# Kernel optimization log

Hardware: AMD Instinct MI355X
Metric: run time of the kernel (lower is better)

Reference implementation:

```python
import jax, jax.numpy as jnp
import numpy as np

B, T, C = 8, 2048, 512   # batch, seq_len, channels (= output_size for residual)
H, K, D = 4, 128, 128    # heads, key_size, per-head value size
KS, DIL = 4, 4           # conv kernel size, dilation = kernal_size**block_id
BAND = 3                 # matrix_band_part num_lower = num_upper = 3
NEG = -10000000.0


def setup_inputs() -> dict:
    key = jax.random.key(0)
    ks = jax.random.split(key, 12)
    s = 0.02
    f32 = jnp.float32
    x = jax.random.normal(ks[0], (B, T, C), f32)
    # per-head q/k/v dense params (stacked over head axis)
    Wq = jax.random.normal(ks[1], (H, C, K), f32) * s
    bq = jnp.zeros((H, K), f32)
    Wk = jax.random.normal(ks[2], (H, C, K), f32) * s
    bk = jnp.zeros((H, K), f32)
    Wv = jax.random.normal(ks[3], (H, C, D), f32) * s
    bv = jnp.zeros((H, D), f32)
    # output combiner Dense(output_size)
    Wo = jax.random.normal(ks[4], (H * D, C), f32) * s
    bo = jnp.zeros((C,), f32)
    # causal dilated Conv1D: kernel layout WIO = (kernel, in, out)
    Wc = jax.random.normal(ks[5], (KS, C, C), f32) * s
    bc = jnp.zeros((C,), f32)
    return {"x": x, "Wq": Wq, "bq": bq, "Wk": Wk, "bk": bk,
            "Wv": Wv, "bv": bv, "Wo": Wo, "bo": bo, "Wc": Wc, "bc": bc}


def reference(x, Wq, bq, Wk, bk, Wv, bv, Wo, bo, Wc, bc):
    # per-head projections: [B,H,T,K/D]
    q = jnp.einsum('btc,hck->bhtk', x, Wq) + bq[None, :, None, :]
    k = jnp.einsum('btc,hck->bhtk', x, Wk) + bk[None, :, None, :]
    v = jnp.einsum('btc,hcd->bhtd', x, Wv) + bv[None, :, None, :]
    # dense scores then band mask (faithful to matrix_band_part + abs>0 mask)
    sim = jnp.einsum('bhtk,bhsk->bhts', q, k) / jnp.sqrt(jnp.float32(K))
    idx = jnp.arange(T)
    band = (jnp.abs(idx[:, None] - idx[None, :]) <= BAND).astype(sim.dtype)
    simb = sim * band
    mask = jnp.where(jnp.abs(simb) > 0.0, 0.0, 1.0).astype(sim.dtype)
    att = jax.nn.softmax(simb + NEG * mask, axis=-1)
    heads = jnp.einsum('bhts,bhsd->bhtd', att, v)          # [B,H,T,D]
    cat = heads.transpose(0, 2, 1, 3).reshape(B, T, H * D)  # concat heads
    out = cat @ Wo + bo                                     # Dense(512)
    # causal dilated conv + relu
    pad = (KS - 1) * DIL
    conv = jax.lax.conv_general_dilated(
        out, Wc, window_strides=(1,), padding=[(pad, 0)],
        rhs_dilation=(DIL,), dimension_numbers=('NWC', 'WIO', 'NWC'))
    conv = jax.nn.relu(conv + bc)
    res = conv + x
    return jnp.where(res >= 0, res, 0.2 * res)  # leaky_relu(alpha=0.2)
```

## Files before the change

### kernel.cpp

```cpp
#include <hip/hip_runtime.h>
#include <math.h>

#define Bb    8
#define Tseq  2048
#define Cch   512
#define Mrows 16384
#define Nqkv  1536

typedef __bf16 bf16x8 __attribute__((ext_vector_type(8)));
typedef __bf16 bf16x4 __attribute__((ext_vector_type(4)));
typedef float  f32x4  __attribute__((ext_vector_type(4)));

__device__ __forceinline__ void gld_lds16(const void* g, void* l) {
  __builtin_amdgcn_global_load_lds(
      (const __attribute__((address_space(1))) unsigned int*)g,
      (__attribute__((address_space(3))) unsigned int*)l, 16, 0, 0);
}

#define SWZ(r, g) (((r) << 6) + ((((g) ^ ((r) & 7))) << 3))


__global__ __launch_bounds__(256, 4) void gemm_qkv_wp_kernel(
    const __bf16* __restrict__ xb, const __bf16* __restrict__ Wqkv_t,
    const float* __restrict__ bq, const float* __restrict__ bk,
    const float* __restrict__ bv, __bf16* __restrict__ qkv,
    const __bf16* __restrict__ Wc_t, const __bf16* __restrict__ Wob,
    __bf16* __restrict__ Wp_bt) {
  __shared__ __align__(16) __bf16 As[64 * 64];
  __shared__ __align__(16) __bf16 Bs[128 * 64];
  const int tid = threadIdx.x;
  const int w = tid >> 6, lane = tid & 63;
  const int wm = w & 1, wn = w >> 1;
  const int lm = lane & 15, quad = lane >> 4;
  const int srow = lane >> 3;
  const int scol = (((lane & 7) ^ srow) << 3);
  const int lid = blockIdx.x;

  const __bf16 *Ap, *Bp;
  __bf16* op;
  int lda, ldo, m0, n0;
  bool dobias;
  if (lid < 3072) {
    const int xcd = lid & 7, chunk = lid >> 3;
    const int idx = xcd * 384 + chunk;
    const int mt = idx / 12, nt = idx - mt * 12;
    m0 = mt * 64; n0 = nt * 128;
    Ap = xb; lda = 512; Bp = Wqkv_t;
    op = qkv; ldo = 1536; dobias = true;
  } else {
    const int l2 = lid - 3072;
    const int z = l2 >> 5;
    const int rest = l2 & 31;
    m0 = (rest >> 2) * 64;
    n0 = (rest & 3) * 128;
    Ap = Wc_t + z * 512; lda = 2048; Bp = Wob;
    op = Wp_bt + z * 512; ldo = 2048; dobias = false;
  }

  f32x4 acc[2][4] = {};
  for (int k0 = 0; k0 < 512; k0 += 64) {
#pragma unroll
    for (int it = 0; it < 2; ++it) {
      const int c = w * 2 + it;
      const int row = c * 8 + srow;
      gld_lds16(Ap + (size_t)(m0 + row) * lda + k0 + scol, &As[c * 512]);
    }
#pragma unroll
    for (int it = 0; it < 4; ++it) {
      const int c = w * 4 + it;
      const int row = c * 8 + srow;
      gld_lds16(Bp + (size_t)(n0 + row) * 512 + k0 + scol, &Bs[c * 512]);
    }
    __syncthreads();
#pragma unroll
    for (int ks = 0; ks < 2; ++ks) {
      bf16x8 af[2], bfr[4];
#pragma unroll
      for (int i = 0; i < 2; ++i)
        af[i] = *(const bf16x8*)&As[SWZ(wm * 32 + i * 16 + lm, ks * 4 + quad)];
#pragma unroll
      for (int j = 0; j < 4; ++j)
        bfr[j] = *(const bf16x8*)&Bs[SWZ(wn * 64 + j * 16 + lm, ks * 4 + quad)];
#pragma unroll
      for (int i = 0; i < 2; ++i)
#pragma unroll
        for (int j = 0; j < 4; ++j)
          acc[i][j] = __builtin_amdgcn_mfma_f32_16x16x32_bf16(af[i], bfr[j], acc[i][j], 0, 0, 0);
    }
    __syncthreads();
  }
#pragma unroll
  for (int j = 0; j < 4; ++j) {
    const int col = n0 + wn * 64 + j * 16 + lm;
    float bias = 0.f;
    if (dobias) {
      const int s = col >> 9;
      const float* bp = (s == 0) ? bq : (s == 1 ? bk : bv);
      bias = bp[col & 511];
    }
#pragma unroll
    for (int i = 0; i < 2; ++i) {
      const int row0 = m0 + wm * 32 + i * 16 + quad * 4;
#pragma unroll
      for (int r = 0; r < 4; ++r)
        op[(size_t)(row0 + r) * ldo + col] = (__bf16)(acc[i][j][r] + bias);
    }
  }
}

__global__ __launch_bounds__(256, 4) void conv_gemm_kernel(
    const __bf16* __restrict__ A,
    const __bf16* __restrict__ Bt,
    const float* __restrict__ bc, const float* __restrict__ bj,
    const float* __restrict__ x, float* __restrict__ out,
    const __bf16* __restrict__ zeros) {
  __shared__ __align__(16) __bf16 As[64 * 64];
  __shared__ __align__(16) __bf16 Bs[128 * 64];
  const int tid = threadIdx.x;
  const int w = tid >> 6, lane = tid & 63;
  const int wm = w & 1, wn = w >> 1;
  const int lm = lane & 15, quad = lane >> 4;
  const int srow = lane >> 3;
  const int scol = (((lane & 7) ^ srow) << 3);
  const int lid = blockIdx.y * 4 + blockIdx.x;
  const int xcd = lid & 7, chunk = lid >> 3;
  const int idx = xcd * 128 + chunk;
  const int mt = idx >> 2, nt = idx & 3;
  const int m0 = mt * 64, n0 = nt * 128;

  f32x4 acc[2][4] = {};
  for (int k0 = 0; k0 < 4 * Cch; k0 += 64) {
    const int jtap = k0 >> 9;
    const int shift = 4 * jtap - 12;
    const int cin0 = k0 & 511;
#pragma unroll
    for (int it = 0; it < 2; ++it) {
      const int c = w * 2 + it;
      const int row = c * 8 + srow;
      const int m = m0 + row;
      const __bf16* src = (((m & (Tseq - 1)) + shift) >= 0)
                              ? A + (size_t)(m + shift) * Cch + cin0 + scol
                              : zeros + scol;
      gld_lds16(src, &As[c * 512]);
    }
#pragma unroll
    for (int it = 0; it < 4; ++it) {
      const int c = w * 4 + it;
      const int row = c * 8 + srow;
      gld_lds16(Bt + (size_t)(n0 + row) * 2048 + k0 + scol, &Bs[c * 512]);
    }
    __syncthreads();
#pragma unroll
    for (int ks = 0; ks < 2; ++ks) {
      bf16x8 af[2], bfr[4];
#pragma unroll
      for (int i = 0; i < 2; ++i)
        af[i] = *(const bf16x8*)&As[SWZ(wm * 32 + i * 16 + lm, ks * 4 + quad)];
#pragma unroll
      for (int j = 0; j < 4; ++j)
        bfr[j] = *(const bf16x8*)&Bs[SWZ(wn * 64 + j * 16 + lm, ks * 4 + quad)];
#pragma unroll
      for (int i = 0; i < 2; ++i)
#pragma unroll
        for (int j = 0; j < 4; ++j)
          acc[i][j] = __builtin_amdgcn_mfma_f32_16x16x32_bf16(af[i], bfr[j], acc[i][j], 0, 0, 0);
    }
    __syncthreads();
  }
#pragma unroll
  for (int j = 0; j < 4; ++j) {
    const int col = n0 + wn * 64 + j * 16 + lm;
    const float bcv = bc[col];
    float suf[4];
    suf[3] = bj[3 * 512 + col];
    suf[2] = suf[3] + bj[2 * 512 + col];
    suf[1] = suf[2] + bj[1 * 512 + col];
    suf[0] = suf[1] + bj[0 * 512 + col];
#pragma unroll
    for (int i = 0; i < 2; ++i) {
      const int row0 = m0 + wm * 32 + i * 16 + quad * 4;
#pragma unroll
      for (int r = 0; r < 4; ++r) {
        const int row = row0 + r;
        const int tl = row & (Tseq - 1);
        int jm = 15 - tl;
        jm = (jm < 0) ? 0 : (jm >> 2);
        float v = acc[i][j][r] + bcv + suf[jm];
        v = fmaxf(v, 0.f);
        v += x[(size_t)row * Cch + col];
        out[(size_t)row * Cch + col] = (v >= 0.f) ? v : 0.2f * v;
      }
    }
  }
}

__global__ __launch_bounds__(256) void attn_band_kernel(
    const __bf16* __restrict__ qkv, __bf16* __restrict__ cat) {
  __shared__ __align__(16) __bf16 ks[70 * 128];
  __shared__ __align__(16) __bf16 vs[70 * 128];
  const int tid = threadIdx.x;
  const int bh = blockIdx.y;
  const int b = bh >> 2, h = bh & 3;
  const int t0 = blockIdx.x * 64;
  for (int c = tid; c < 70 * 16; c += 256) {
    const int row = c >> 4, chunk = c & 15;
    int s = t0 - 3 + row;
    s = (s < 0) ? 0 : ((s > Tseq - 1) ? Tseq - 1 : s);
    const __bf16* src = qkv + ((size_t)(b * Tseq + s)) * Nqkv + 512 + h * 128 + chunk * 8;
    *(bf16x8*)&ks[row * 128 + chunk * 8] = *(const bf16x8*)src;
    *(bf16x8*)&vs[row * 128 + chunk * 8] = *(const bf16x8*)(src + 512);
  }
  __syncthreads();
  const int g = tid & 15, grp = tid >> 4;
  const int d0 = g * 8;
  const float scale = 0.08838834764831845f;
#pragma unroll
  for (int tt = 0; tt < 4; ++tt) {
    const int tl = grp * 4 + tt;
    const int t = t0 + tl;
    bf16x8 qv = *(const bf16x8*)(qkv + ((size_t)(b * Tseq + t)) * Nqkv + h * 128 + d0);
    float score[7];
#pragma unroll
    for (int i = 0; i < 7; ++i) {
      const int s = t - 3 + i;
      const bool valid = (s >= 0) && (s < Tseq);
      bf16x8 kv = *(const bf16x8*)&ks[(tl + i) * 128 + d0];
      float p = 0.f;
#pragma unroll
      for (int e = 0; e < 8; ++e) p += (float)qv[e] * (float)kv[e];
      p += __shfl_xor(p, 1);
      p += __shfl_xor(p, 2);
      p += __shfl_xor(p, 4);
      p += __shfl_xor(p, 8);
      score[i] = valid ? p * scale : -1e30f;
    }
    float mx = score[0];
#pragma unroll
    for (int i = 1; i < 7; ++i) mx = fmaxf(mx, score[i]);
    float wgt[7], denom = 0.f;
#pragma unroll
    for (int i = 0; i < 7; ++i) {
      wgt[i] = (score[i] > -1e29f) ? expf(score[i] - mx) : 0.f;
      denom += wgt[i];
    }
    const float inv = 1.f / denom;
    float o[8] = {};
#pragma unroll
    for (int i = 0; i < 7; ++i) {
      bf16x8 vv = *(const bf16x8*)&vs[(tl + i) * 128 + d0];
#pragma unroll
      for (int e = 0; e < 8; ++e) o[e] += wgt[i] * (float)vv[e];
    }
    bf16x8 ov;
#pragma unroll
    for (int e = 0; e < 8; ++e) ov[e] = (__bf16)(o[e] * inv);
    *(bf16x8*)(cat + ((size_t)(b * Tseq + t)) * Cch + h * 128 + d0) = ov;
  }
}

#define PREP_A 8192
#define PREP_B 8960
#define PREP_C 9984
#define PREP_D 10240
#define PREP_E 10241
#define PREP_N 10273

__global__ __launch_bounds__(256) void prep_kernel(
    const float* __restrict__ x, const float* __restrict__ Wq,
    const float* __restrict__ Wk, const float* __restrict__ Wv,
    const float* __restrict__ Wo, const float* __restrict__ Wc,
    const float* __restrict__ bo,
    __bf16* __restrict__ xb, __bf16* __restrict__ Wqkv_t,
    __bf16* __restrict__ Wc_t, __bf16* __restrict__ Wob,
    float* __restrict__ bj, __bf16* __restrict__ zeros) {
  __shared__ float sArr[32][33];
  __shared__ float red[256];
  const int bid = blockIdx.x;
  const int tid = threadIdx.x;
  if (bid < PREP_A) {
    const size_t i = ((size_t)bid * 256 + tid) * 4;
    float4 v = *(const float4*)(x + i);
    bf16x4 o;
    o[0] = (__bf16)v.x; o[1] = (__bf16)v.y; o[2] = (__bf16)v.z; o[3] = (__bf16)v.w;
    *(bf16x4*)(xb + i) = o;
  } else if (bid < PREP_B) {
    const int l = bid - PREP_A;
    const int bx = l & 3, by = (l >> 2) & 15, z = l >> 6;
    const int sgrp = z >> 2, h = z & 3;
    const float* src = ((sgrp == 0) ? Wq : (sgrp == 1) ? Wk : Wv) + h * (512 * 128);
    __bf16* dst = Wqkv_t + (size_t)z * 128 * 512;
    const int tx = tid & 31, ty = tid >> 5;
    const int c0 = bx * 32, r0 = by * 32;
#pragma unroll
    for (int rr = 0; rr < 4; ++rr)
      sArr[ty + rr * 8][tx] = src[(size_t)(r0 + ty + rr * 8) * 128 + c0 + tx];
    __syncthreads();
#pragma unroll
    for (int rr = 0; rr < 4; ++rr)
      dst[(size_t)(c0 + ty + rr * 8) * 512 + r0 + tx] = (__bf16)sArr[tx][ty + rr * 8];
  } else if (bid < PREP_C) {
    const int l = bid - PREP_B;
    const int bx = l & 15, by = l >> 4;
    const int tx = tid & 31, ty = tid >> 5;
    const int c0 = bx * 32, r0 = by * 32;
#pragma unroll
    for (int rr = 0; rr < 4; ++rr)
      sArr[ty + rr * 8][tx] = Wc[(size_t)(r0 + ty + rr * 8) * 512 + c0 + tx];
    __syncthreads();
#pragma unroll
    for (int rr = 0; rr < 4; ++rr)
      Wc_t[(size_t)(c0 + ty + rr * 8) * 2048 + r0 + tx] = (__bf16)sArr[tx][ty + rr * 8];
  } else if (bid < PREP_D) {
    const int l = bid - PREP_C;
    const size_t i = ((size_t)l * 256 + tid) * 4;
    float4 v = *(const float4*)(Wo + i);
    bf16x4 o;
    o[0] = (__bf16)v.x; o[1] = (__bf16)v.y; o[2] = (__bf16)v.z; o[3] = (__bf16)v.w;
    *(bf16x4*)(Wob + i) = o;
  } else if (bid < PREP_E) {
    bf16x8 zero = {};
    *(bf16x8*)(zeros + tid * 8) = zero;
  } else {
    const int l = bid - PREP_E;
    const int j = l >> 3, nb = l & 7;
    const int n = nb * 64 + (tid & 63);
    const int cig = tid >> 6;
    const float* base = Wc + ((size_t)j * 512 + cig * 128) * 512 + n;
    float acc = 0.f;
#pragma unroll 8
    for (int ci = 0; ci < 128; ++ci) acc += bo[cig * 128 + ci] * base[(size_t)ci * 512];
    red[tid] = acc;
    __syncthreads();
    if (tid < 64)
      bj[j * 512 + n] = red[tid] + red[tid + 64] + red[tid + 128] + red[tid + 192];
  }
}

extern "C" void kernel_launch(void* const* d_in, const int* in_sizes, int n_in,
                              void* d_out, int out_size, void* d_ws, size_t ws_size,
                              hipStream_t stream) {
  const float* x  = (const float*)d_in[0];
  const float* Wq = (const float*)d_in[1];
  const float* bq = (const float*)d_in[2];
  const float* Wk = (const float*)d_in[3];
  const float* bk = (const float*)d_in[4];
  const float* Wv = (const float*)d_in[5];
  const float* bv = (const float*)d_in[6];
  const float* Wo = (const float*)d_in[7];
  const float* bo = (const float*)d_in[8];
  const float* Wc = (const float*)d_in[9];
  const float* bc = (const float*)d_in[10];
  float* out = (float*)d_out;

  char* p = (char*)d_ws;
  __bf16* xb     = (__bf16*)p;  p += (size_t)Mrows * Cch * 2;
  __bf16* qkv    = (__bf16*)p;  p += (size_t)Mrows * Nqkv * 2;
  __bf16* catb   = (__bf16*)p;  p += (size_t)Mrows * Cch * 2;
  __bf16* Wqkv_t = (__bf16*)p;  p += (size_t)Nqkv * Cch * 2;
  __bf16* Wc_t   = (__bf16*)p;  p += (size_t)Cch * 2048 * 2;
  __bf16* Wob    = (__bf16*)p;  p += (size_t)Cch * Cch * 2;
  __bf16* Wp_bt  = (__bf16*)p;  p += (size_t)Cch * 2048 * 2;
  float*  bj     = (float*)p;   p += 4 * Cch * 4;
  __bf16* zeros  = (__bf16*)p;  p += 4096;

  prep_kernel<<<PREP_N, 256, 0, stream>>>(x, Wq, Wk, Wv, Wo, Wc, bo,
                                          xb, Wqkv_t, Wc_t, Wob, bj, zeros);

  gemm_qkv_wp_kernel<<<3200, 256, 0, stream>>>(xb, Wqkv_t, bq, bk, bv, qkv,
                                               Wc_t, Wob, Wp_bt);

  attn_band_kernel<<<dim3(Tseq / 64, Bb * 4), 256, 0, stream>>>(qkv, catb);

  conv_gemm_kernel<<<dim3(4, 256), 256, 0, stream>>>(
      catb, Wp_bt, bc, bj, x, out, zeros);
}
```

Before: 209.6 us.

## Fuse QKV projection with banded attention to keep Q/K/V in LDS

Merges the QKV GEMM and the band-attention kernel into one kernel. Each block computes Q for a 64-row strip and K/V for that strip plus a halo of neighbouring rows, per head pair, and writes them straight into shared memory before running the 7-wide softmax. This removes the round trip of the full qkv tensor through global memory and one kernel launch. In exchange it recomputes the K/V halo rows, uses far more LDS per block, drops occupancy to 2 blocks per CU, and launches only 512 attention blocks that each run a long serial chain of GEMMs.

```diff
diff --git a/kernel.cpp b/kernel.cpp
--- a/kernel.cpp
+++ b/kernel.cpp
@@ -19,92 +19,233 @@
 
 #define SWZ(r, g) (((r) << 6) + ((((g) ^ ((r) & 7))) << 3))
 
-
-__global__ __launch_bounds__(256, 4) void gemm_qkv_wp_kernel(
+__global__ __launch_bounds__(256, 2) void qkv_attn_kernel(
     const __bf16* __restrict__ xb, const __bf16* __restrict__ Wqkv_t,
     const float* __restrict__ bq, const float* __restrict__ bk,
-    const float* __restrict__ bv, __bf16* __restrict__ qkv,
+    const float* __restrict__ bv, __bf16* __restrict__ catb,
     const __bf16* __restrict__ Wc_t, const __bf16* __restrict__ Wob,
     __bf16* __restrict__ Wp_bt) {
-  __shared__ __align__(16) __bf16 As[64 * 64];
+  __shared__ __align__(16) __bf16 As[80 * 64];
   __shared__ __align__(16) __bf16 Bs[128 * 64];
+  __shared__ __align__(16) __bf16 qs[64 * 128];
+  __shared__ __align__(16) __bf16 ksh[72 * 128];
+  __shared__ __align__(16) __bf16 vsh[72 * 128];
   const int tid = threadIdx.x;
   const int w = tid >> 6, lane = tid & 63;
-  const int wm = w & 1, wn = w >> 1;
   const int lm = lane & 15, quad = lane >> 4;
   const int srow = lane >> 3;
   const int scol = (((lane & 7) ^ srow) << 3);
   const int lid = blockIdx.x;
 
-  const __bf16 *Ap, *Bp;
-  __bf16* op;
-  int lda, ldo, m0, n0;
-  bool dobias;
-  if (lid < 3072) {
-    const int xcd = lid & 7, chunk = lid >> 3;
-    const int idx = xcd * 384 + chunk;
-    const int mt = idx / 12, nt = idx - mt * 12;
-    m0 = mt * 64; n0 = nt * 128;
-    Ap = xb; lda = 512; Bp = Wqkv_t;
-    op = qkv; ldo = 1536; dobias = true;
-  } else {
-    const int l2 = lid - 3072;
-    const int z = l2 >> 5;
-    const int rest = l2 & 31;
-    m0 = (rest >> 2) * 64;
-    n0 = (rest & 3) * 128;
-    Ap = Wc_t + z * 512; lda = 2048; Bp = Wob;
-    op = Wp_bt + z * 512; ldo = 2048; dobias = false;
+  if (lid >= 512) {
+    const int l2 = lid - 512;
+    const int z = l2 >> 5, rest = l2 & 31;
+    const int m0 = (rest >> 2) * 64, n0 = (rest & 3) * 128;
+    const __bf16* Ap = Wc_t + z * 512;
+    const int wm = w & 1, wn = w >> 1;
+    f32x4 acc[2][4] = {};
+    for (int k0 = 0; k0 < 512; k0 += 64) {
+#pragma unroll
+      for (int it = 0; it < 2; ++it) {
+        const int c = w * 2 + it;
+        gld_lds16(Ap + (size_t)(m0 + c * 8 + srow) * 2048 + k0 + scol, &As[c * 512]);
+      }
+#pragma unroll
+      for (int it = 0; it < 4; ++it) {
+        const int c = w * 4 + it;
+        gld_lds16(Wob + (size_t)(n0 + c * 8 + srow) * 512 + k0 + scol, &Bs[c * 512]);
+      }
+      __syncthreads();
+#pragma unroll
+      for (int kss = 0; kss < 2; ++kss) {
+        bf16x8 af[2], bfr[4];
+#pragma unroll
+        for (int i = 0; i < 2; ++i)
+          af[i] = *(const bf16x8*)&As[SWZ(wm * 32 + i * 16 + lm, kss * 4 + quad)];
+#pragma unroll
+        for (int j = 0; j < 4; ++j)
+          bfr[j] = *(const bf16x8*)&Bs[SWZ(wn * 64 + j * 16 + lm, kss * 4 + quad)];
+#pragma unroll
+        for (int i = 0; i < 2; ++i)
+#pragma unroll
+          for (int j = 0; j < 4; ++j)
+            acc[i][j] = __builtin_amdgcn_mfma_f32_16x16x32_bf16(af[i], bfr[j], acc[i][j], 0, 0, 0);
+      }
+      __syncthreads();
+    }
+#pragma unroll
+    for (int j = 0; j < 4; ++j) {
+      const int col = n0 + wn * 64 + j * 16 + lm;
+#pragma unroll
+      for (int i = 0; i < 2; ++i) {
+        const int row0 = m0 + wm * 32 + i * 16 + quad * 4;
+#pragma unroll
+        for (int r = 0; r < 4; ++r)
+          Wp_bt[(size_t)(row0 + r) * 2048 + z * 512 + col] = (__bf16)acc[i][j][r];
+      }
+    }
+    return;
   }
 
-  f32x4 acc[2][4] = {};
-  for (int k0 = 0; k0 < 512; k0 += 64) {
-#pragma unroll
-    for (int it = 0; it < 2; ++it) {
-      const int c = w * 2 + it;
-      const int row = c * 8 + srow;
-      gld_lds16(Ap + (size_t)(m0 + row) * lda + k0 + scol, &As[c * 512]);
-    }
-#pragma unroll
-    for (int it = 0; it < 4; ++it) {
-      const int c = w * 4 + it;
-      const int row = c * 8 + srow;
-      gld_lds16(Bp + (size_t)(n0 + row) * 512 + k0 + scol, &Bs[c * 512]);
-    }
-    __syncthreads();
-#pragma unroll
-    for (int ks = 0; ks < 2; ++ks) {
-      bf16x8 af[2], bfr[4];
-#pragma unroll
-      for (int i = 0; i < 2; ++i)
-        af[i] = *(const bf16x8*)&As[SWZ(wm * 32 + i * 16 + lm, ks * 4 + quad)];
-#pragma unroll
-      for (int j = 0; j < 4; ++j)
-        bfr[j] = *(const bf16x8*)&Bs[SWZ(wn * 64 + j * 16 + lm, ks * 4 + quad)];
-#pragma unroll
-      for (int i = 0; i < 2; ++i)
-#pragma unroll
-        for (int j = 0; j < 4; ++j)
-          acc[i][j] = __builtin_amdgcn_mfma_f32_16x16x32_bf16(af[i], bfr[j], acc[i][j], 0, 0, 0);
-    }
-    __syncthreads();
-  }
-#pragma unroll
-  for (int j = 0; j < 4; ++j) {
-    const int col = n0 + wn * 64 + j * 16 + lm;
-    float bias = 0.f;
-    if (dobias) {
-      const int s = col >> 9;
-      const float* bp = (s == 0) ? bq : (s == 1 ? bk : bv);
-      bias = bp[col & 511];
-    }
-#pragma unroll
-    for (int i = 0; i < 2; ++i) {
-      const int row0 = m0 + wm * 32 + i * 16 + quad * 4;
-#pragma unroll
-      for (int r = 0; r < 4; ++r)
-        op[(size_t)(row0 + r) * ldo + col] = (__bf16)(acc[i][j][r] + bias);
-    }
+  const int idx = (lid & 7) * 64 + (lid >> 3);
+  const int strip = idx >> 1, hp = idx & 1;
+  const int b = strip >> 5;
+  const int tloc0 = (strip & 31) * 64;
+  const int m0 = strip * 64;
+  const __bf16* Arow0 = xb + (size_t)m0 * 512;
+
+  for (int hh = 0; hh < 2; ++hh) {
+    const int h = hp * 2 + hh;
+    {
+      const __bf16* Bp = Wqkv_t + (size_t)h * 128 * 512;
+      const int wm = w & 1, wn = w >> 1;
+      f32x4 acc[2][4] = {};
+      for (int k0 = 0; k0 < 512; k0 += 64) {
+#pragma unroll
+        for (int it = 0; it < 2; ++it) {
+          const int c = w * 2 + it;
+          gld_lds16(Arow0 + (size_t)(c * 8 + srow) * 512 + k0 + scol, &As[c * 512]);
+        }
+#pragma unroll
+        for (int it = 0; it < 4; ++it) {
+          const int c = w * 4 + it;
+          gld_lds16(Bp + (size_t)(c * 8 + srow) * 512 + k0 + scol, &Bs[c * 512]);
+        }
+        __syncthreads();
+#pragma unroll
+        for (int kss = 0; kss < 2; ++kss) {
+          bf16x8 af[2], bfr[4];
+#pragma unroll
+          for (int i = 0; i < 2; ++i)
+            af[i] = *(const bf16x8*)&As[SWZ(wm * 32 + i * 16 + lm, kss * 4 + quad)];
+#pragma unroll
+          for (int j = 0; j < 4; ++j)
+            bfr[j] = *(const bf16x8*)&Bs[SWZ(wn * 64 + j * 16 + lm, kss * 4 + quad)];
+#pragma unroll
+          for (int i = 0; i < 2; ++i)
+#pragma unroll
+            for (int j = 0; j < 4; ++j)
+              acc[i][j] = __builtin_amdgcn_mfma_f32_16x16x32_bf16(af[i], bfr[j], acc[i][j], 0, 0, 0);
+        }
+        __syncthreads();
+      }
+#pragma unroll
+      for (int j = 0; j < 4; ++j) {
+        const int col = wn * 64 + j * 16 + lm;
+        const float bias = bq[h * 128 + col];
+#pragma unroll
+        for (int i = 0; i < 2; ++i) {
+          const int row0 = wm * 32 + i * 16 + quad * 4;
+#pragma unroll
+          for (int r = 0; r < 4; ++r)
+            qs[(row0 + r) * 128 + col] = (__bf16)(acc[i][j][r] + bias);
+        }
+      }
+    }
+#pragma unroll 1
+    for (int kv = 0; kv < 2; ++kv) {
+      const __bf16* Bp = Wqkv_t + (size_t)(4 + kv * 4 + h) * 128 * 512;
+      const float* bias_p = kv ? bv : bk;
+      __bf16* dst = kv ? vsh : ksh;
+      const int wn2 = w;
+      f32x4 acc[5][2] = {};
+      for (int k0 = 0; k0 < 512; k0 += 64) {
+#pragma unroll
+        for (int it = 0; it < 3; ++it) {
+          const int c = w + it * 4;
+          if (c < 10) {
+            int tl = tloc0 - 4 + c * 8 + srow;
+            tl = tl < 0 ? 0 : (tl > 2047 ? 2047 : tl);
+            gld_lds16(xb + ((size_t)(b * 2048 + tl)) * 512 + k0 + scol, &As[c * 512]);
+          }
+        }
+#pragma unroll
+        for (int it = 0; it < 4; ++it) {
+          const int c = w * 4 + it;
+          gld_lds16(Bp + (size_t)(c * 8 + srow) * 512 + k0 + scol, &Bs[c * 512]);
+        }
+        __syncthreads();
+#pragma unroll
+        for (int kss = 0; kss < 2; ++kss) {
+          bf16x8 af[5], bfr[2];
+#pragma unroll
+          for (int i = 0; i < 5; ++i)
+            af[i] = *(const bf16x8*)&As[SWZ(i * 16 + lm, kss * 4 + quad)];
+#pragma unroll
+          for (int j = 0; j < 2; ++j)
+            bfr[j] = *(const bf16x8*)&Bs[SWZ(wn2 * 32 + j * 16 + lm, kss * 4 + quad)];
+#pragma unroll
+          for (int i = 0; i < 5; ++i)
+#pragma unroll
+            for (int j = 0; j < 2; ++j)
+              acc[i][j] = __builtin_amdgcn_mfma_f32_16x16x32_bf16(af[i], bfr[j], acc[i][j], 0, 0, 0);
+        }
+        __syncthreads();
+      }
+#pragma unroll
+      for (int j = 0; j < 2; ++j) {
+        const int col = wn2 * 32 + j * 16 + lm;
+        const float bias = bias_p[h * 128 + col];
+#pragma unroll
+        for (int i = 0; i < 5; ++i) {
+          const int row0 = i * 16 + quad * 4;
+#pragma unroll
+          for (int r = 0; r < 4; ++r) {
+            const int row = row0 + r;
+            if (row < 72)
+              dst[row * 128 + col] = (__bf16)(acc[i][j][r] + bias);
+          }
+        }
+      }
+    }
+    __syncthreads();
+    {
+      const int g = tid & 15, grp = tid >> 4;
+      const int d0 = g * 8;
+      const float scale = 0.08838834764831845f;
+#pragma unroll
+      for (int tt = 0; tt < 4; ++tt) {
+        const int tl = grp * 4 + tt;
+        bf16x8 qv = *(const bf16x8*)&qs[tl * 128 + d0];
+        float score[7];
+#pragma unroll
+        for (int i = 0; i < 7; ++i) {
+          const int s = tloc0 + tl - 3 + i;
+          const bool valid = (s >= 0) && (s < Tseq);
+          bf16x8 kvv = *(const bf16x8*)&ksh[(tl + 1 + i) * 128 + d0];
+          float p = 0.f;
+#pragma unroll
+          for (int e = 0; e < 8; ++e) p += (float)qv[e] * (float)kvv[e];
+          p += __shfl_xor(p, 1);
+          p += __shfl_xor(p, 2);
+          p += __shfl_xor(p, 4);
+          p += __shfl_xor(p, 8);
+          score[i] = valid ? p * scale : -1e30f;
+        }
+        float mx = score[0];
+#pragma unroll
+        for (int i = 1; i < 7; ++i) mx = fmaxf(mx, score[i]);
+        float wgt[7], denom = 0.f;
+#pragma unroll
+        for (int i = 0; i < 7; ++i) {
+          wgt[i] = (score[i] > -1e29f) ? expf(score[i] - mx) : 0.f;
+          denom += wgt[i];
+        }
+        const float inv = 1.f / denom;
+        float o[8] = {};
+#pragma unroll
+        for (int i = 0; i < 7; ++i) {
+          bf16x8 vv = *(const bf16x8*)&vsh[(tl + 1 + i) * 128 + d0];
+#pragma unroll
+          for (int e = 0; e < 8; ++e) o[e] += wgt[i] * (float)vv[e];
+        }
+        bf16x8 ov;
+#pragma unroll
+        for (int e = 0; e < 8; ++e) ov[e] = (__bf16)(o[e] * inv);
+        *(bf16x8*)(catb + ((size_t)(m0 + tl)) * Cch + h * 128 + d0) = ov;
+      }
+    }
+    __syncthreads();
   }
 }
 
@@ -191,70 +332,6 @@
         out[(size_t)row * Cch + col] = (v >= 0.f) ? v : 0.2f * v;
       }
     }
-  }
-}
-
-__global__ __launch_bounds__(256) void attn_band_kernel(
-    const __bf16* __restrict__ qkv, __bf16* __restrict__ cat) {
-  __shared__ __align__(16) __bf16 ks[70 * 128];
-  __shared__ __align__(16) __bf16 vs[70 * 128];
-  const int tid = threadIdx.x;
-  const int bh = blockIdx.y;
-  const int b = bh >> 2, h = bh & 3;
-  const int t0 = blockIdx.x * 64;
-  for (int c = tid; c < 70 * 16; c += 256) {
-    const int row = c >> 4, chunk = c & 15;
-    int s = t0 - 3 + row;
-    s = (s < 0) ? 0 : ((s > Tseq - 1) ? Tseq - 1 : s);
-    const __bf16* src = qkv + ((size_t)(b * Tseq + s)) * Nqkv + 512 + h * 128 + chunk * 8;
-    *(bf16x8*)&ks[row * 128 + chunk * 8] = *(const bf16x8*)src;
-    *(bf16x8*)&vs[row * 128 + chunk * 8] = *(const bf16x8*)(src + 512);
-  }
-  __syncthreads();
-  const int g = tid & 15, grp = tid >> 4;
-  const int d0 = g * 8;
-  const float scale = 0.08838834764831845f;
-#pragma unroll
-  for (int tt = 0; tt < 4; ++tt) {
-    const int tl = grp * 4 + tt;
-    const int t = t0 + tl;
-    bf16x8 qv = *(const bf16x8*)(qkv + ((size_t)(b * Tseq + t)) * Nqkv + h * 128 + d0);
-    float score[7];
-#pragma unroll
-    for (int i = 0; i < 7; ++i) {
-      const int s = t - 3 + i;
-      const bool valid = (s >= 0) && (s < Tseq);
-      bf16x8 kv = *(const bf16x8*)&ks[(tl + i) * 128 + d0];
-      float p = 0.f;
-#pragma unroll
-      for (int e = 0; e < 8; ++e) p += (float)qv[e] * (float)kv[e];
-      p += __shfl_xor(p, 1);
-      p += __shfl_xor(p, 2);
-      p += __shfl_xor(p, 4);
-      p += __shfl_xor(p, 8);
-      score[i] = valid ? p * scale : -1e30f;
-    }
-    float mx = score[0];
-#pragma unroll
-    for (int i = 1; i < 7; ++i) mx = fmaxf(mx, score[i]);
-    float wgt[7], denom = 0.f;
-#pragma unroll
-    for (int i = 0; i < 7; ++i) {
-      wgt[i] = (score[i] > -1e29f) ? expf(score[i] - mx) : 0.f;
-      denom += wgt[i];
-    }
-    const float inv = 1.f / denom;
-    float o[8] = {};
-#pragma unroll
-    for (int i = 0; i < 7; ++i) {
-      bf16x8 vv = *(const bf16x8*)&vs[(tl + i) * 128 + d0];
-#pragma unroll
-      for (int e = 0; e < 8; ++e) o[e] += wgt[i] * (float)vv[e];
-    }
-    bf16x8 ov;
-#pragma unroll
-    for (int e = 0; e < 8; ++e) ov[e] = (__bf16)(o[e] * inv);
-    *(bf16x8*)(cat + ((size_t)(b * Tseq + t)) * Cch + h * 128 + d0) = ov;
   }
 }
 
@@ -362,14 +439,13 @@
   __bf16* Wp_bt  = (__bf16*)p;  p += (size_t)Cch * 2048 * 2;
   float*  bj     = (float*)p;   p += 4 * Cch * 4;
   __bf16* zeros  = (__bf16*)p;  p += 4096;
+  (void)qkv;
 
   prep_kernel<<<PREP_N, 256, 0, stream>>>(x, Wq, Wk, Wv, Wo, Wc, bo,
                                           xb, Wqkv_t, Wc_t, Wob, bj, zeros);
 
-  gemm_qkv_wp_kernel<<<3200, 256, 0, stream>>>(xb, Wqkv_t, bq, bk, bv, qkv,
-                                               Wc_t, Wob, Wp_bt);
-
-  attn_band_kernel<<<dim3(Tseq / 64, Bb * 4), 256, 0, stream>>>(qkv, catb);
+  qkv_attn_kernel<<<640, 256, 0, stream>>>(xb, Wqkv_t, bq, bk, bv, catb,
+                                           Wc_t, Wob, Wp_bt);
 
   conv_gemm_kernel<<<dim3(4, 256), 256, 0, stream>>>(
       catb, Wp_bt, bc, bj, x, out, zeros);
```

After: 235.3 us. 12.3% more time.
